# Optimization experiments

Measured on AMD Instinct MI355X. Metric: run time of the kernel, lower is better.

Reference implementation:

```python
import jax, jax.numpy as jnp
import numpy as np

B, D, K = 4096, 1024, 32

def setup_inputs() -> dict:
    key = jax.random.key(0)
    k1, k2, k3, k4 = jax.random.split(key, 4)
    e1 = jax.random.normal(k1, (B, D), dtype=jnp.float32)
    e2 = jax.random.normal(k2, (B, D), dtype=jnp.float32)
    W = jax.random.normal(k3, (K, D, D), dtype=jnp.float32)
    V = jax.random.normal(k4, (2 * D, K), dtype=jnp.float32)
    b = jnp.zeros((D,), dtype=jnp.float32)
    return {"e1": e1, "e2": e2, "W": W, "V": V, "b": b}

def reference(e1, e2, W, V, b):
    batch = e1.shape[0]
    k = W.shape[0]
    # Per-slice bilinear form: btp[i, n] = sum_d e2[n,d] * (e1[n] @ W[i])[d] + sum(b)
    # (b is added elementwise before the axis-1 sum in the original, i.e. +sum(b))
    btp = jnp.einsum('bd,kde,be->kb', e1, W, e2) + jnp.sum(b)  # (k, B)
    # Original concatenates k (B,)-vectors along axis 0 then reshapes to (B, k);
    # reproduce that exact (interleaving) layout.
    btp = btp.reshape(batch, k)
    ff = jnp.concatenate([e1, e2], axis=-1) @ V  # (B, k)
    return jnp.tanh(btp + ff)
```

## Files before the change

kernel.cpp:

```cpp
#include <hip/hip_runtime.h>

#define B_SZ 4096
#define D_SZ 1024
#define K_SZ 32

typedef _Float16 h16x8 __attribute__((ext_vector_type(8)));
typedef float f32x4 __attribute__((ext_vector_type(4)));
typedef float f32x2 __attribute__((ext_vector_type(2)));
typedef unsigned int u32x2 __attribute__((ext_vector_type(2)));
typedef unsigned int u32x4 __attribute__((ext_vector_type(4)));
typedef unsigned short u16x4 __attribute__((ext_vector_type(4)));

#define GLOAD16(gp, sp) __builtin_amdgcn_global_load_lds( \
    (const __attribute__((address_space(1))) void*)(gp),  \
    (__attribute__((address_space(3))) void*)(sp), 16, 0, 0)

__device__ __forceinline__ void split1(float x, _Float16& h, _Float16& l) {
    h = (_Float16)x;
    l = (_Float16)((x - (float)h) * 2048.0f);
}

__global__ __launch_bounds__(256)
void ntl_prep_w(const float* __restrict__ W,
                _Float16* __restrict__ Wh, _Float16* __restrict__ Wl) {
    __shared__ float tile[64 * 69];
    const int bid = blockIdx.x;
    const int k  = bid >> 8;
    const int d0 = ((bid >> 4) & 15) << 6;
    const int e0 = (bid & 15) << 6;
    const int t  = threadIdx.x;
    const int r  = t >> 4;
    const int c4 = (t & 15) << 2;

    const float* src = W + ((size_t)k * D_SZ + d0) * D_SZ + e0;
    #pragma unroll
    for (int p = 0; p < 4; ++p) {
        f32x4 v = *(const f32x4*)(src + (size_t)(p * 16 + r) * D_SZ + c4);
        float* dst = &tile[(p * 16 + r) * 69 + c4];
        dst[0] = v[0]; dst[1] = v[1]; dst[2] = v[2]; dst[3] = v[3];
    }
    __syncthreads();
    #pragma unroll
    for (int p = 0; p < 4; ++p) {
        const int e = p * 16 + r;
        u16x4 hh, ll;
        #pragma unroll
        for (int q = 0; q < 4; ++q) {
            float v = tile[(c4 + q) * 69 + e];
            _Float16 h, l;
            split1(v, h, l);
            hh[q] = __builtin_bit_cast(unsigned short, h);
            ll[q] = __builtin_bit_cast(unsigned short, l);
        }
        const size_t o = ((size_t)k * D_SZ + e0 + e) * D_SZ + d0 + c4;
        *(u16x4*)(Wh + o) = hh;
        *(u16x4*)(Wl + o) = ll;
    }
}

__global__ __launch_bounds__(256)
void ntl_prep_e(const float* __restrict__ e1,
                _Float16* __restrict__ eh, _Float16* __restrict__ el) {
    const size_t i = ((size_t)blockIdx.x * 256 + threadIdx.x) * 4;
    f32x4 v = *(const f32x4*)(e1 + i);
    u16x4 hh, ll;
    #pragma unroll
    for (int q = 0; q < 4; ++q) {
        _Float16 h, l;
        split1(v[q], h, l);
        hh[q] = __builtin_bit_cast(unsigned short, h);
        ll[q] = __builtin_bit_cast(unsigned short, l);
    }
    *(u16x4*)(eh + i) = hh;
    *(u16x4*)(el + i) = ll;
}

__global__ __launch_bounds__(256, 2)
void ntl_bilinear2(const _Float16* __restrict__ eh, const _Float16* __restrict__ el,
                   const _Float16* __restrict__ Wh, const _Float16* __restrict__ Wl,
                   const float* __restrict__ e2, float* __restrict__ out) {
    __shared__ __align__(16) _Float16 lds[4 * 128 * 64];
    char* const base = (char*)lds;

    const int bid = blockIdx.x;
    const int k   = bid >> 8;
    const int rem = bid & 255;
    const int b0  = (rem >> 3) * 128;
    const int e0  = (rem & 7) * 128;

    const int t  = threadIdx.x;
    const int l  = t & 63;
    const int w  = t >> 6;
    const int wr = (w >> 1) * 64;
    const int wc = (w & 1) * 64;
    const int lrow = l & 15;
    const int lq   = l >> 4;

    f32x4 acc1[4][4];
    f32x4 acc2[4][4];
    #pragma unroll
    for (int m = 0; m < 4; ++m)
        #pragma unroll
        for (int n = 0; n < 4; ++n) {
            acc1[m][n] = f32x4{0.f, 0.f, 0.f, 0.f};
            acc2[m][n] = f32x4{0.f, 0.f, 0.f, 0.f};
        }

    const int srow  = l >> 3;
    const int gslot = (l & 7) ^ srow;
    const size_t aoff = (size_t)(b0 + w * 8 + srow) * D_SZ + gslot * 8;
    const size_t boff = ((size_t)k * D_SZ + e0 + w * 8 + srow) * D_SZ + gslot * 8;
    const _Float16* gAh = eh + aoff;
    const _Float16* gAl = el + aoff;
    const _Float16* gBh = Wh + boff;
    const _Float16* gBl = Wl + boff;

    for (int kt = 0; kt < D_SZ / 64; ++kt) {
        const int d0 = kt * 64;
        #pragma unroll
        for (int p = 0; p < 4; ++p) {
            const size_t ro = (size_t)p * 32 * D_SZ + d0;
            char* sb_ = base + p * 4096 + w * 1024;
            GLOAD16(gAh + ro, sb_);
            GLOAD16(gAl + ro, sb_ + 16384);
            GLOAD16(gBh + ro, sb_ + 32768);
            GLOAD16(gBl + ro, sb_ + 49152);
        }
        __syncthreads();

        #pragma unroll
        for (int kk = 0; kk < 2; ++kk) {
            h16x8 a_h[4], a_l[4];
            #pragma unroll
            for (int m = 0; m < 4; ++m) {
                const int r = wr + m * 16 + lrow;
                const int off = r * 128 + (((kk * 4 + lq) ^ (r & 7)) << 4);
                a_h[m] = *(const h16x8*)(base + off);
                a_l[m] = *(const h16x8*)(base + 16384 + off);
            }
            #pragma unroll
            for (int n = 0; n < 4; ++n) {
                const int r = wc + n * 16 + lrow;
                const int off = r * 128 + (((kk * 4 + lq) ^ (r & 7)) << 4);
                h16x8 b_h = *(const h16x8*)(base + 32768 + off);
                h16x8 b_l = *(const h16x8*)(base + 49152 + off);
                #pragma unroll
                for (int m = 0; m < 4; ++m) {
                    acc1[m][n] = __builtin_amdgcn_mfma_f32_16x16x32_f16(a_h[m], b_h, acc1[m][n], 0, 0, 0);
                    acc2[m][n] = __builtin_amdgcn_mfma_f32_16x16x32_f16(a_h[m], b_l, acc2[m][n], 0, 0, 0);
                    acc2[m][n] = __builtin_amdgcn_mfma_f32_16x16x32_f16(a_l[m], b_h, acc2[m][n], 0, 0, 0);
                }
            }
        }
        __syncthreads();
    }

    float rsum[16];
    #pragma unroll
    for (int i = 0; i < 16; ++i) rsum[i] = 0.f;

    #pragma unroll
    for (int m = 0; m < 4; ++m) {
        #pragma unroll
        for (int n = 0; n < 4; ++n) {
            const int col = e0 + wc + n * 16 + lrow;
            #pragma unroll
            for (int j = 0; j < 4; ++j) {
                const int row = b0 + wr + m * 16 + lq * 4 + j;
                float tv = acc1[m][n][j] + acc2[m][n][j] * (1.0f / 2048.0f);
                rsum[m * 4 + j] += tv * e2[(size_t)row * D_SZ + col];
            }
        }
    }

    #pragma unroll
    for (int i = 0; i < 16; ++i) {
        float v = rsum[i];
        v += __shfl_xor(v, 1, 16);
        v += __shfl_xor(v, 2, 16);
        v += __shfl_xor(v, 4, 16);
        v += __shfl_xor(v, 8, 16);
        if (lrow == 0) {
            const int row = b0 + wr + (i >> 2) * 16 + lq * 4 + (i & 3);
            atomicAdd(out + (size_t)k * B_SZ + row, v);
        }
    }
}

__device__ __forceinline__ int swz_fb(int row, int byte_in_row) {
    int slot = byte_in_row >> 4;
    int in   = byte_in_row & 15;
    return row * 128 + (((slot ^ (row & 7)) << 4) | in);
}
__device__ __forceinline__ void split_fb(float x, unsigned short& h, unsigned short& l) {
    _Float16 hf = (_Float16)x;
    float hff = (float)hf;
    _Float16 lf = (_Float16)((x - hff) * 2048.0f);
    h = __builtin_bit_cast(unsigned short, hf);
    l = __builtin_bit_cast(unsigned short, lf);
}
__global__ __launch_bounds__(256, 2)
void ntl_bilinear_fb(const float* __restrict__ e1, const float* __restrict__ e2,
                     const float* __restrict__ W, float* __restrict__ out) {
    __shared__ __align__(16) char smem[65536];
    char* const Ah = smem;
    char* const Al = smem + 16384;
    char* const Bh = smem + 32768;
    char* const Bl = smem + 49152;
    const int bid = blockIdx.x;
    const int k   = bid >> 8;
    const int rem = bid & 255;
    const int b0  = (rem >> 3) * 128;
    const int e0  = (rem & 7) * 128;
    const int t  = threadIdx.x;
    const int l  = t & 63;
    const int w  = t >> 6;
    const int wr = (w >> 1) * 64;
    const int wc = (w & 1) * 64;
    const int lrow = l & 15;
    const int lq   = l >> 4;
    f32x4 acc1[4][4], acc2[4][4];
    #pragma unroll
    for (int m = 0; m < 4; ++m)
        #pragma unroll
        for (int n = 0; n < 4; ++n) {
            acc1[m][n] = f32x4{0.f, 0.f, 0.f, 0.f};
            acc2[m][n] = f32x4{0.f, 0.f, 0.f, 0.f};
        }
    const int sa_row = t >> 4;
    const int sa_cg  = (t & 15) * 4;
    const int sb_e   = t & 127;
    const int sb_dg  = t >> 7;
    const float* const e1b = e1 + (size_t)b0 * D_SZ;
    const float* const wb  = W + ((size_t)k * D_SZ) * D_SZ + e0 + sb_e;
    for (int kt = 0; kt < D_SZ / 64; ++kt) {
        const int d0 = kt * 64;
        #pragma unroll
        for (int p = 0; p < 8; ++p) {
            const int r = sa_row + p * 16;
            f32x4 v = *(const f32x4*)(e1b + (size_t)r * D_SZ + d0 + sa_cg);
            unsigned short hh[4], ll[4];
            #pragma unroll
            for (int q = 0; q < 4; ++q) split_fb(v[q], hh[q], ll[q]);
            u32x2 hv = { (unsigned)hh[0] | ((unsigned)hh[1] << 16),
                         (unsigned)hh[2] | ((unsigned)hh[3] << 16) };
            u32x2 lv = { (unsigned)ll[0] | ((unsigned)ll[1] << 16),
                         (unsigned)ll[2] | ((unsigned)ll[3] << 16) };
            const int ad = swz_fb(r, sa_cg * 2);
            *(u32x2*)(Ah + ad) = hv;
            *(u32x2*)(Al + ad) = lv;
        }
        {
            const float* ws2 = wb + (size_t)(d0 + sb_dg * 32) * D_SZ;
            #pragma unroll
            for (int g = 0; g < 4; ++g) {
                unsigned short hh[8], ll[8];
                #pragma unroll
                for (int i = 0; i < 8; ++i)
                    split_fb(ws2[(size_t)(g * 8 + i) * D_SZ], hh[i], ll[i]);
                u32x4 hv = { (unsigned)hh[0] | ((unsigned)hh[1] << 16),
                             (unsigned)hh[2] | ((unsigned)hh[3] << 16),
                             (unsigned)hh[4] | ((unsigned)hh[5] << 16),
                             (unsigned)hh[6] | ((unsigned)hh[7] << 16) };
                u32x4 lv = { (unsigned)ll[0] | ((unsigned)ll[1] << 16),
                             (unsigned)ll[2] | ((unsigned)ll[3] << 16),
                             (unsigned)ll[4] | ((unsigned)ll[5] << 16),
                             (unsigned)ll[6] | ((unsigned)ll[7] << 16) };
                const int ad = swz_fb(sb_e, (sb_dg * 32 + g * 8) * 2);
                *(u32x4*)(Bh + ad) = hv;
                *(u32x4*)(Bl + ad) = lv;
            }
        }
        __syncthreads();
        #pragma unroll
        for (int kk = 0; kk < 2; ++kk) {
            const int kb = kk * 64 + lq * 16;
            h16x8 a_h[4], a_l[4];
            #pragma unroll
            for (int m = 0; m < 4; ++m) {
                const int ad = swz_fb(wr + m * 16 + lrow, kb);
                a_h[m] = *(const h16x8*)(Ah + ad);
                a_l[m] = *(const h16x8*)(Al + ad);
            }
            #pragma unroll
            for (int n = 0; n < 4; ++n) {
                const int bd = swz_fb(wc + n * 16 + lrow, kb);
                h16x8 b_h = *(const h16x8*)(Bh + bd);
                h16x8 b_l = *(const h16x8*)(Bl + bd);
                #pragma unroll
                for (int m = 0; m < 4; ++m) {
                    acc1[m][n] = __builtin_amdgcn_mfma_f32_16x16x32_f16(a_h[m], b_h, acc1[m][n], 0, 0, 0);
                    acc2[m][n] = __builtin_amdgcn_mfma_f32_16x16x32_f16(a_h[m], b_l, acc2[m][n], 0, 0, 0);
                    acc2[m][n] = __builtin_amdgcn_mfma_f32_16x16x32_f16(a_l[m], b_h, acc2[m][n], 0, 0, 0);
                }
            }
        }
        __syncthreads();
    }
    float rsum[16];
    #pragma unroll
    for (int i = 0; i < 16; ++i) rsum[i] = 0.f;
    #pragma unroll
    for (int m = 0; m < 4; ++m) {
        #pragma unroll
        for (int n = 0; n < 4; ++n) {
            const int col = e0 + wc + n * 16 + lrow;
            #pragma unroll
            for (int j = 0; j < 4; ++j) {
                const int row = b0 + wr + m * 16 + lq * 4 + j;
                float tv = acc1[m][n][j] + acc2[m][n][j] * (1.0f / 2048.0f);
                rsum[m * 4 + j] += tv * e2[(size_t)row * D_SZ + col];
            }
        }
    }
    #pragma unroll
    for (int i = 0; i < 16; ++i) {
        float v = rsum[i];
        v += __shfl_xor(v, 1, 16);
        v += __shfl_xor(v, 2, 16);
        v += __shfl_xor(v, 4, 16);
        v += __shfl_xor(v, 8, 16);
        if (lrow == 0) {
            const int row = b0 + wr + (i >> 2) * 16 + lq * 4 + (i & 3);
            atomicAdd(out + (size_t)k * B_SZ + row, v);
        }
    }
}

__global__ __launch_bounds__(256)
void ntl_ff(const float* __restrict__ e1, const float* __restrict__ e2,
            const float* __restrict__ V, float* __restrict__ out) {
    __shared__ float vt[32 * 258];
    const int t  = threadIdx.x;
    const int c  = t & 31;
    const int rl = t >> 5;
    const int r  = blockIdx.x * 8 + rl;
    float acc = 0.f;
    for (int j0 = 0; j0 < 2 * D_SZ; j0 += 256) {
        __syncthreads();
        #pragma unroll
        for (int i = 0; i < 32; ++i) {
            const int f = i * 256 + t;
            vt[(f & 31) * 258 + (f >> 5)] = V[(size_t)j0 * K_SZ + f];
        }
        __syncthreads();
        const float* src = (j0 < D_SZ) ? (e1 + (size_t)r * D_SZ + j0)
                                       : (e2 + (size_t)r * D_SZ + (j0 - D_SZ));
        #pragma unroll 8
        for (int jj = 0; jj < 256; jj += 2) {
            f32x2 a  = *(const f32x2*)(src + jj);
            f32x2 vv = *(const f32x2*)(&vt[c * 258 + jj]);
            acc += a[0] * vv[0] + a[1] * vv[1];
        }
    }
    out[(size_t)r * K_SZ + c] += acc;
}

__global__ void ntl_sumb(const float* __restrict__ b, float* __restrict__ ws) {
    __shared__ float red[256];
    const int t = threadIdx.x;
    red[t] = b[t] + b[t + 256] + b[t + 512] + b[t + 768];
    __syncthreads();
    for (int s = 128; s > 0; s >>= 1) {
        if (t < s) red[t] += red[t + s];
        __syncthreads();
    }
    if (t == 0) ws[0] = red[0];
}

__global__ void ntl_tanh(float* __restrict__ out, const float* __restrict__ ws) {
    const int p = blockIdx.x * 256 + threadIdx.x;
    out[p] = tanhf(out[p] + ws[0]);
}

extern "C" void kernel_launch(void* const* d_in, const int* in_sizes, int n_in,
                              void* d_out, int out_size, void* d_ws, size_t ws_size,
                              hipStream_t stream) {
    const float* e1 = (const float*)d_in[0];
    const float* e2 = (const float*)d_in[1];
    const float* W  = (const float*)d_in[2];
    const float* V  = (const float*)d_in[3];
    const float* b  = (const float*)d_in[4];
    float* out = (float*)d_out;

    const size_t WT = (size_t)K_SZ * D_SZ * D_SZ;
    const size_t ET = (size_t)B_SZ * D_SZ;
    const size_t need = (2 * WT + 2 * ET) * sizeof(_Float16) + 16;

    hipMemsetAsync(d_out, 0, (size_t)B_SZ * K_SZ * sizeof(float), stream);

    if (ws_size >= need) {
        _Float16* Wh = (_Float16*)d_ws;
        _Float16* Wl = Wh + WT;
        _Float16* eh = Wl + WT;
        _Float16* el = eh + ET;
        float* sb = (float*)(el + ET);
        ntl_sumb<<<1, 256, 0, stream>>>(b, sb);
        ntl_prep_w<<<dim3(K_SZ * 256), dim3(256), 0, stream>>>(W, Wh, Wl);
        ntl_prep_e<<<dim3((int)(ET / 1024)), dim3(256), 0, stream>>>(e1, eh, el);
        ntl_bilinear2<<<dim3(K_SZ * 256), dim3(256), 0, stream>>>(eh, el, Wh, Wl, e2, out);
        ntl_ff<<<dim3(B_SZ / 8), dim3(256), 0, stream>>>(e1, e2, V, out);
        ntl_tanh<<<dim3((B_SZ * K_SZ) / 256), dim3(256), 0, stream>>>(out, sb);
    } else {
        float* sb = (float*)d_ws;
        ntl_sumb<<<1, 256, 0, stream>>>(b, sb);
        ntl_bilinear_fb<<<dim3(K_SZ * 256), dim3(256), 0, stream>>>(e1, e2, W, out);
        ntl_ff<<<dim3(B_SZ / 8), dim3(256), 0, stream>>>(e1, e2, V, out);
        ntl_tanh<<<dim3((B_SZ * K_SZ) / 256), dim3(256), 0, stream>>>(out, sb);
    }
}
```

Measured before the change: 820.2 us.

## Rewrite bilinear GEMM with 256x128 tiles, 32x32 MFMA and double-buffered prefetch

Replaces the 128x128, 256-thread bilinear kernel with a 512-thread kernel. Each block computes a 256x128 tile using 32x32x16 MFMA instructions. B tiles are double-buffered in LDS through direct global-to-LDS loads, and the next A tile is prefetched into registers while the current step computes. Blocks are also remapped so that each XCD works on a fixed range of batch rows, which should improve L2 reuse. The aim is to cut global traffic per FLOP and hide load latency, at the cost of a 128 KB LDS footprint that likely allows only one block per CU.

```diff
diff --git a/kernel.cpp b/kernel.cpp
--- a/kernel.cpp
+++ b/kernel.cpp
@@ -3,8 +3,10 @@
 #define B_SZ 4096
 #define D_SZ 1024
 #define K_SZ 32
+#define NT   16
 
 typedef _Float16 h16x8 __attribute__((ext_vector_type(8)));
+typedef float f32x16 __attribute__((ext_vector_type(16)));
 typedef float f32x4 __attribute__((ext_vector_type(4)));
 typedef float f32x2 __attribute__((ext_vector_type(2)));
 typedef unsigned int u32x2 __attribute__((ext_vector_type(2)));
@@ -75,114 +77,162 @@
     *(u16x4*)(el + i) = ll;
 }
 
-__global__ __launch_bounds__(256, 2)
-void ntl_bilinear2(const _Float16* __restrict__ eh, const _Float16* __restrict__ el,
+__global__ __launch_bounds__(512, 2)
+void ntl_bilinear4(const _Float16* __restrict__ eh, const _Float16* __restrict__ el,
                    const _Float16* __restrict__ Wh, const _Float16* __restrict__ Wl,
                    const float* __restrict__ e2, float* __restrict__ out) {
-    __shared__ __align__(16) _Float16 lds[4 * 128 * 64];
-    char* const base = (char*)lds;
-
-    const int bid = blockIdx.x;
-    const int k   = bid >> 8;
-    const int rem = bid & 255;
-    const int b0  = (rem >> 3) * 128;
-    const int e0  = (rem & 7) * 128;
-
-    const int t  = threadIdx.x;
-    const int l  = t & 63;
-    const int w  = t >> 6;
-    const int wr = (w >> 1) * 64;
-    const int wc = (w & 1) * 64;
-    const int lrow = l & 15;
-    const int lq   = l >> 4;
-
-    f32x4 acc1[4][4];
-    f32x4 acc2[4][4];
-    #pragma unroll
-    for (int m = 0; m < 4; ++m)
-        #pragma unroll
-        for (int n = 0; n < 4; ++n) {
-            acc1[m][n] = f32x4{0.f, 0.f, 0.f, 0.f};
-            acc2[m][n] = f32x4{0.f, 0.f, 0.f, 0.f};
-        }
-
-    const int srow  = l >> 3;
-    const int gslot = (l & 7) ^ srow;
-    const size_t aoff = (size_t)(b0 + w * 8 + srow) * D_SZ + gslot * 8;
-    const size_t boff = ((size_t)k * D_SZ + e0 + w * 8 + srow) * D_SZ + gslot * 8;
-    const _Float16* gAh = eh + aoff;
-    const _Float16* gAl = el + aoff;
-    const _Float16* gBh = Wh + boff;
-    const _Float16* gBl = Wl + boff;
-
-    for (int kt = 0; kt < D_SZ / 64; ++kt) {
-        const int d0 = kt * 64;
-        #pragma unroll
-        for (int p = 0; p < 4; ++p) {
-            const size_t ro = (size_t)p * 32 * D_SZ + d0;
-            char* sb_ = base + p * 4096 + w * 1024;
-            GLOAD16(gAh + ro, sb_);
-            GLOAD16(gAl + ro, sb_ + 16384);
-            GLOAD16(gBh + ro, sb_ + 32768);
-            GLOAD16(gBl + ro, sb_ + 49152);
-        }
-        __syncthreads();
-
-        #pragma unroll
-        for (int kk = 0; kk < 2; ++kk) {
-            h16x8 a_h[4], a_l[4];
-            #pragma unroll
-            for (int m = 0; m < 4; ++m) {
-                const int r = wr + m * 16 + lrow;
-                const int off = r * 128 + (((kk * 4 + lq) ^ (r & 7)) << 4);
-                a_h[m] = *(const h16x8*)(base + off);
-                a_l[m] = *(const h16x8*)(base + 16384 + off);
-            }
-            #pragma unroll
-            for (int n = 0; n < 4; ++n) {
-                const int r = wc + n * 16 + lrow;
-                const int off = r * 128 + (((kk * 4 + lq) ^ (r & 7)) << 4);
-                h16x8 b_h = *(const h16x8*)(base + 32768 + off);
-                h16x8 b_l = *(const h16x8*)(base + 49152 + off);
+    __shared__ __align__(16) char lds[131072];
+
+    const int bid   = blockIdx.x;
+    const int xcd   = bid & 7;
+    const int idx   = bid >> 3;
+    const int e_t   = idx & 7;
+    const int b_sub = (idx >> 3) & 1;
+    const int k     = idx >> 4;
+    const int b0    = (xcd * 2 + b_sub) * 256;
+    const int e0    = e_t * 128;
+
+    const int t    = threadIdx.x;
+    const int l    = t & 63;
+    const int w    = t >> 6;
+    const int wrow = (w >> 1) * 64;
+    const int wcol = (w & 1) * 64;
+    const int l31  = l & 31;
+    const int h5   = l >> 5;
+    const int srow = l >> 3;
+    const int sl   = l & 7;
+
+    f32x16 acc1[2][2];
+    f32x16 acc2[2][2];
+    #pragma unroll
+    for (int m = 0; m < 2; ++m)
+        #pragma unroll
+        for (int n = 0; n < 2; ++n) {
+            #pragma unroll
+            for (int j = 0; j < 16; ++j) { acc1[m][n][j] = 0.f; acc2[m][n][j] = 0.f; }
+        }
+
+    const size_t arow = (size_t)(b0 + w * 32 + srow) * D_SZ + sl * 8;
+    const _Float16* gAh = eh + arow;
+    const _Float16* gAl = el + arow;
+    const int awOff = (w * 32 + srow) * 128 + ((sl ^ srow) << 4);
+
+    const int gslot = sl ^ srow;
+    const _Float16* gB = (w < 4 ? Wh : Wl) +
+        ((size_t)k * D_SZ + e0 + (w & 3) * 32 + srow) * D_SZ + gslot * 8;
+    const int bOff = (w >= 4 ? 16384 : 0) + (w & 3) * 4096;
+
+    u32x4 arH[4], arL[4];
+
+    {
+        char* bset = lds + 65536;
+        #pragma unroll
+        for (int i = 0; i < 4; ++i)
+            GLOAD16(gB + (size_t)i * 8 * D_SZ, bset + bOff + i * 1024);
+        #pragma unroll
+        for (int i = 0; i < 4; ++i) {
+            arH[i] = *(const u32x4*)(gAh + (size_t)i * 8 * D_SZ);
+            arL[i] = *(const u32x4*)(gAl + (size_t)i * 8 * D_SZ);
+        }
+    }
+
+    for (int kt = 0; kt < NT; ++kt) {
+        if (kt) {
+            __builtin_amdgcn_s_barrier();
+            __builtin_amdgcn_sched_barrier(0);
+        }
+        asm volatile("s_waitcnt vmcnt(0)" ::: "memory");
+        __builtin_amdgcn_sched_barrier(0);
+
+        #pragma unroll
+        for (int i = 0; i < 4; ++i) {
+            *(u32x4*)(lds + awOff + i * 1024)         = arH[i];
+            *(u32x4*)(lds + 32768 + awOff + i * 1024) = arL[i];
+        }
+
+        if (kt + 1 < NT) {
+            const size_t dn = (size_t)(kt + 1) * 64;
+            char* bset = lds + 65536 + (((kt + 1) & 1) << 15);
+            #pragma unroll
+            for (int i = 0; i < 4; ++i)
+                GLOAD16(gB + (size_t)i * 8 * D_SZ + dn, bset + bOff + i * 1024);
+            #pragma unroll
+            for (int i = 0; i < 4; ++i) {
+                arH[i] = *(const u32x4*)(gAh + (size_t)i * 8 * D_SZ + dn);
+                arL[i] = *(const u32x4*)(gAl + (size_t)i * 8 * D_SZ + dn);
+            }
+        }
+
+        asm volatile("s_waitcnt lgkmcnt(0)" ::: "memory");
+        __builtin_amdgcn_sched_barrier(0);
+        __builtin_amdgcn_s_barrier();
+        __builtin_amdgcn_sched_barrier(0);
+
+        const char* Bh_ = lds + 65536 + ((kt & 1) << 15);
+        const char* Bl_ = Bh_ + 16384;
+
+        #pragma unroll
+        for (int ks = 0; ks < 4; ++ks) {
+            h16x8 ah[2], al[2], bh[2], bl[2];
+            #pragma unroll
+            for (int m = 0; m < 2; ++m) {
+                const int r = wrow + m * 32 + l31;
+                const int off = r * 128 + (((ks * 2 + h5) ^ (r & 7)) << 4);
+                ah[m] = *(const h16x8*)(lds + off);
+                al[m] = *(const h16x8*)(lds + 32768 + off);
+            }
+            #pragma unroll
+            for (int n = 0; n < 2; ++n) {
+                const int r = wcol + n * 32 + l31;
+                const int off = r * 128 + (((ks * 2 + h5) ^ (r & 7)) << 4);
+                bh[n] = *(const h16x8*)(Bh_ + off);
+                bl[n] = *(const h16x8*)(Bl_ + off);
+            }
+            #pragma unroll
+            for (int m = 0; m < 2; ++m)
                 #pragma unroll
-                for (int m = 0; m < 4; ++m) {
-                    acc1[m][n] = __builtin_amdgcn_mfma_f32_16x16x32_f16(a_h[m], b_h, acc1[m][n], 0, 0, 0);
-                    acc2[m][n] = __builtin_amdgcn_mfma_f32_16x16x32_f16(a_h[m], b_l, acc2[m][n], 0, 0, 0);
-                    acc2[m][n] = __builtin_amdgcn_mfma_f32_16x16x32_f16(a_l[m], b_h, acc2[m][n], 0, 0, 0);
+                for (int n = 0; n < 2; ++n) {
+                    acc1[m][n] = __builtin_amdgcn_mfma_f32_32x32x16_f16(ah[m], bh[n], acc1[m][n], 0, 0, 0);
+                    acc2[m][n] = __builtin_amdgcn_mfma_f32_32x32x16_f16(ah[m], bl[n], acc2[m][n], 0, 0, 0);
+                    acc2[m][n] = __builtin_amdgcn_mfma_f32_32x32x16_f16(al[m], bh[n], acc2[m][n], 0, 0, 0);
                 }
-            }
-        }
-        __syncthreads();
-    }
-
-    float rsum[16];
-    #pragma unroll
-    for (int i = 0; i < 16; ++i) rsum[i] = 0.f;
-
-    #pragma unroll
-    for (int m = 0; m < 4; ++m) {
-        #pragma unroll
-        for (int n = 0; n < 4; ++n) {
-            const int col = e0 + wc + n * 16 + lrow;
-            #pragma unroll
-            for (int j = 0; j < 4; ++j) {
-                const int row = b0 + wr + m * 16 + lq * 4 + j;
-                float tv = acc1[m][n][j] + acc2[m][n][j] * (1.0f / 2048.0f);
-                rsum[m * 4 + j] += tv * e2[(size_t)row * D_SZ + col];
-            }
-        }
-    }
-
-    #pragma unroll
-    for (int i = 0; i < 16; ++i) {
-        float v = rsum[i];
-        v += __shfl_xor(v, 1, 16);
-        v += __shfl_xor(v, 2, 16);
-        v += __shfl_xor(v, 4, 16);
-        v += __shfl_xor(v, 8, 16);
-        if (lrow == 0) {
-            const int row = b0 + wr + (i >> 2) * 16 + lq * 4 + (i & 3);
-            atomicAdd(out + (size_t)k * B_SZ + row, v);
+        }
+    }
+
+    float rsum[2][16];
+    #pragma unroll
+    for (int m = 0; m < 2; ++m)
+        #pragma unroll
+        for (int rg = 0; rg < 16; ++rg) rsum[m][rg] = 0.f;
+
+    #pragma unroll
+    for (int m = 0; m < 2; ++m) {
+        #pragma unroll
+        for (int n = 0; n < 2; ++n) {
+            #pragma unroll
+            for (int rg = 0; rg < 16; ++rg) {
+                const int rowl = wrow + m * 32 + (rg & 3) + 8 * (rg >> 2) + 4 * h5;
+                const int col  = e0 + wcol + n * 32 + l31;
+                float tv = acc1[m][n][rg] + acc2[m][n][rg] * (1.0f / 2048.0f);
+                rsum[m][rg] += tv * e2[(size_t)(b0 + rowl) * D_SZ + col];
+            }
+        }
+    }
+
+    #pragma unroll
+    for (int m = 0; m < 2; ++m) {
+        #pragma unroll
+        for (int rg = 0; rg < 16; ++rg) {
+            float v = rsum[m][rg];
+            v += __shfl_xor(v, 1, 32);
+            v += __shfl_xor(v, 2, 32);
+            v += __shfl_xor(v, 4, 32);
+            v += __shfl_xor(v, 8, 32);
+            v += __shfl_xor(v, 16, 32);
+            if (l31 == 0) {
+                const int rowl = wrow + m * 32 + (rg & 3) + 8 * (rg >> 2) + 4 * h5;
+                atomicAdd(out + (size_t)k * B_SZ + b0 + rowl, v);
+            }
         }
     }
 }
@@ -233,7 +283,7 @@
     const int sb_dg  = t >> 7;
     const float* const e1b = e1 + (size_t)b0 * D_SZ;
     const float* const wb  = W + ((size_t)k * D_SZ) * D_SZ + e0 + sb_e;
-    for (int kt = 0; kt < D_SZ / 64; ++kt) {
+    for (int kt = 0; kt < NT; ++kt) {
         const int d0 = kt * 64;
         #pragma unroll
         for (int p = 0; p < 8; ++p) {
@@ -241,7 +291,7 @@
             f32x4 v = *(const f32x4*)(e1b + (size_t)r * D_SZ + d0 + sa_cg);
             unsigned short hh[4], ll[4];
             #pragma unroll
-            for (int q = 0; q < 4; ++q) split_fb(v[q], hh[q], ll[q]);
+            for (int qq = 0; qq < 4; ++qq) split_fb(v[qq], hh[qq], ll[qq]);
             u32x2 hv = { (unsigned)hh[0] | ((unsigned)hh[1] << 16),
                          (unsigned)hh[2] | ((unsigned)hh[3] << 16) };
             u32x2 lv = { (unsigned)ll[0] | ((unsigned)ll[1] << 16),
@@ -253,11 +303,11 @@
         {
             const float* ws2 = wb + (size_t)(d0 + sb_dg * 32) * D_SZ;
             #pragma unroll
-            for (int g = 0; g < 4; ++g) {
+            for (int gg = 0; gg < 4; ++gg) {
                 unsigned short hh[8], ll[8];
                 #pragma unroll
                 for (int i = 0; i < 8; ++i)
-                    split_fb(ws2[(size_t)(g * 8 + i) * D_SZ], hh[i], ll[i]);
+                    split_fb(ws2[(size_t)(gg * 8 + i) * D_SZ], hh[i], ll[i]);
                 u32x4 hv = { (unsigned)hh[0] | ((unsigned)hh[1] << 16),
                              (unsigned)hh[2] | ((unsigned)hh[3] << 16),
                              (unsigned)hh[4] | ((unsigned)hh[5] << 16),
@@ -266,7 +316,7 @@
                              (unsigned)ll[2] | ((unsigned)ll[3] << 16),
                              (unsigned)ll[4] | ((unsigned)ll[5] << 16),
                              (unsigned)ll[6] | ((unsigned)ll[7] << 16) };
-                const int ad = swz_fb(sb_e, (sb_dg * 32 + g * 8) * 2);
+                const int ad = swz_fb(sb_e, (sb_dg * 32 + gg * 8) * 2);
                 *(u32x4*)(Bh + ad) = hv;
                 *(u32x4*)(Bl + ad) = lv;
             }
@@ -398,7 +448,7 @@
         ntl_sumb<<<1, 256, 0, stream>>>(b, sb);
         ntl_prep_w<<<dim3(K_SZ * 256), dim3(256), 0, stream>>>(W, Wh, Wl);
         ntl_prep_e<<<dim3((int)(ET / 1024)), dim3(256), 0, stream>>>(e1, eh, el);
-        ntl_bilinear2<<<dim3(K_SZ * 256), dim3(256), 0, stream>>>(eh, el, Wh, Wl, e2, out);
+        ntl_bilinear4<<<dim3(4096), dim3(512), 0, stream>>>(eh, el, Wh, Wl, e2, out);
         ntl_ff<<<dim3(B_SZ / 8), dim3(256), 0, stream>>>(e1, e2, V, out);
         ntl_tanh<<<dim3((B_SZ * K_SZ) / 256), dim3(256), 0, stream>>>(out, sb);
     } else {
```

After: 947.0 us. 1.15x slower.

## Double-buffer LDS in bilinear GEMM with 32-wide K tiles and async prefetch

Applied to the files above, without the earlier changes.

Replaces the single-buffered 64-wide K-step loop with a double-buffered pipeline over 32-wide K tiles. Each LDS row now packs the hi and lo halves together, and the next-but-one tile is prefetched while the current one is computed, using manual vmcnt waits and raw s_barriers. The aim is to overlap global-to-LDS loads with MFMA work instead of stalling on __syncthreads every step. In exchange it doubles the number of barriers and iterations. The hand-tuned waitcnt must match the exact number of outstanding loads, or the pipeline will read data that has not arrived yet.

```diff
diff --git a/kernel.cpp b/kernel.cpp
--- a/kernel.cpp
+++ b/kernel.cpp
@@ -3,6 +3,7 @@
 #define B_SZ 4096
 #define D_SZ 1024
 #define K_SZ 32
+#define NT   32
 
 typedef _Float16 h16x8 __attribute__((ext_vector_type(8)));
 typedef float f32x4 __attribute__((ext_vector_type(4)));
@@ -76,11 +77,10 @@
 }
 
 __global__ __launch_bounds__(256, 2)
-void ntl_bilinear2(const _Float16* __restrict__ eh, const _Float16* __restrict__ el,
+void ntl_bilinear6(const _Float16* __restrict__ eh, const _Float16* __restrict__ el,
                    const _Float16* __restrict__ Wh, const _Float16* __restrict__ Wl,
                    const float* __restrict__ e2, float* __restrict__ out) {
-    __shared__ __align__(16) _Float16 lds[4 * 128 * 64];
-    char* const base = (char*)lds;
+    __shared__ __align__(16) char lds[65536];
 
     const int bid = blockIdx.x;
     const int k   = bid >> 8;
@@ -106,54 +106,93 @@
             acc2[m][n] = f32x4{0.f, 0.f, 0.f, 0.f};
         }
 
-    const int srow  = l >> 3;
-    const int gslot = (l & 7) ^ srow;
-    const size_t aoff = (size_t)(b0 + w * 8 + srow) * D_SZ + gslot * 8;
-    const size_t boff = ((size_t)k * D_SZ + e0 + w * 8 + srow) * D_SZ + gslot * 8;
-    const _Float16* gAh = eh + aoff;
-    const _Float16* gAl = el + aoff;
-    const _Float16* gBh = Wh + boff;
-    const _Float16* gBl = Wl + boff;
-
-    for (int kt = 0; kt < D_SZ / 64; ++kt) {
-        const int d0 = kt * 64;
-        #pragma unroll
-        for (int p = 0; p < 4; ++p) {
-            const size_t ro = (size_t)p * 32 * D_SZ + d0;
-            char* sb_ = base + p * 4096 + w * 1024;
-            GLOAD16(gAh + ro, sb_);
-            GLOAD16(gAl + ro, sb_ + 16384);
-            GLOAD16(gBh + ro, sb_ + 32768);
-            GLOAD16(gBl + ro, sb_ + 49152);
-        }
-        __syncthreads();
-
-        #pragma unroll
-        for (int kk = 0; kk < 2; ++kk) {
-            h16x8 a_h[4], a_l[4];
+    const int sline = l >> 3;
+    const int sx    = (l & 7) ^ sline;
+    const int hl    = sx >> 2;
+    const int lqs   = sx & 3;
+
+    const _Float16* aBase = hl ? el : eh;
+    const _Float16* bBase = hl ? Wl : Wh;
+    const _Float16* gA[4];
+    const _Float16* gB[4];
+    #pragma unroll
+    for (int i = 0; i < 4; ++i) {
+        const int row = w * 32 + i * 8 + sline;
+        gA[i] = aBase + (size_t)(b0 + row) * D_SZ + lqs * 8;
+        gB[i] = bBase + ((size_t)k * D_SZ + e0 + row) * D_SZ + lqs * 8;
+    }
+    const int sOff = w * 32 * 128;
+
+#define STAGE(bufsel, ktv) do {                                          \
+        char* bb = lds + ((bufsel) ? 32768 : 0);                         \
+        const size_t kb = (size_t)(ktv) * 32;                            \
+        GLOAD16(gA[0] + kb, bb + sOff);                                  \
+        GLOAD16(gA[1] + kb, bb + sOff + 1024);                           \
+        GLOAD16(gA[2] + kb, bb + sOff + 2048);                           \
+        GLOAD16(gA[3] + kb, bb + sOff + 3072);                           \
+        GLOAD16(gB[0] + kb, bb + 16384 + sOff);                          \
+        GLOAD16(gB[1] + kb, bb + 16384 + sOff + 1024);                   \
+        GLOAD16(gB[2] + kb, bb + 16384 + sOff + 2048);                   \
+        GLOAD16(gB[3] + kb, bb + 16384 + sOff + 3072);                   \
+    } while (0)
+
+    int aoffH[4], aoffL[4], boffH[4], boffL[4];
+    #pragma unroll
+    for (int m = 0; m < 4; ++m) {
+        const int r = wr + m * 16 + lrow;
+        aoffH[m] = r * 128 + ((lq       ^ (r & 7)) << 4);
+        aoffL[m] = r * 128 + (((4 | lq) ^ (r & 7)) << 4);
+    }
+    #pragma unroll
+    for (int n = 0; n < 4; ++n) {
+        const int r = wc + n * 16 + lrow;
+        boffH[n] = 16384 + r * 128 + ((lq       ^ (r & 7)) << 4);
+        boffL[n] = 16384 + r * 128 + (((4 | lq) ^ (r & 7)) << 4);
+    }
+
+    STAGE(0, 0);
+    STAGE(1, 1);
+
+    for (int kt = 0; kt < NT; ++kt) {
+        if (kt < NT - 1) {
+            asm volatile("s_waitcnt vmcnt(8)" ::: "memory");
+        } else {
+            asm volatile("s_waitcnt vmcnt(0)" ::: "memory");
+        }
+        __builtin_amdgcn_sched_barrier(0);
+        __builtin_amdgcn_s_barrier();
+        __builtin_amdgcn_sched_barrier(0);
+
+        const char* buf = lds + ((kt & 1) ? 32768 : 0);
+
+        h16x8 a_h[4], a_l[4];
+        #pragma unroll
+        for (int m = 0; m < 4; ++m) {
+            a_h[m] = *(const h16x8*)(buf + aoffH[m]);
+            a_l[m] = *(const h16x8*)(buf + aoffL[m]);
+        }
+        #pragma unroll
+        for (int n = 0; n < 4; ++n) {
+            h16x8 b_h = *(const h16x8*)(buf + boffH[n]);
+            h16x8 b_l = *(const h16x8*)(buf + boffL[n]);
             #pragma unroll
             for (int m = 0; m < 4; ++m) {
-                const int r = wr + m * 16 + lrow;
-                const int off = r * 128 + (((kk * 4 + lq) ^ (r & 7)) << 4);
-                a_h[m] = *(const h16x8*)(base + off);
-                a_l[m] = *(const h16x8*)(base + 16384 + off);
-            }
-            #pragma unroll
-            for (int n = 0; n < 4; ++n) {
-                const int r = wc + n * 16 + lrow;
-                const int off = r * 128 + (((kk * 4 + lq) ^ (r & 7)) << 4);
-                h16x8 b_h = *(const h16x8*)(base + 32768 + off);
-                h16x8 b_l = *(const h16x8*)(base + 49152 + off);
-                #pragma unroll
-                for (int m = 0; m < 4; ++m) {
-                    acc1[m][n] = __builtin_amdgcn_mfma_f32_16x16x32_f16(a_h[m], b_h, acc1[m][n], 0, 0, 0);
-                    acc2[m][n] = __builtin_amdgcn_mfma_f32_16x16x32_f16(a_h[m], b_l, acc2[m][n], 0, 0, 0);
-                    acc2[m][n] = __builtin_amdgcn_mfma_f32_16x16x32_f16(a_l[m], b_h, acc2[m][n], 0, 0, 0);
-                }
-            }
-        }
-        __syncthreads();
-    }
+                acc1[m][n] = __builtin_amdgcn_mfma_f32_16x16x32_f16(a_h[m], b_h, acc1[m][n], 0, 0, 0);
+                acc2[m][n] = __builtin_amdgcn_mfma_f32_16x16x32_f16(a_h[m], b_l, acc2[m][n], 0, 0, 0);
+                acc2[m][n] = __builtin_amdgcn_mfma_f32_16x16x32_f16(a_l[m], b_h, acc2[m][n], 0, 0, 0);
+            }
+        }
+
+        __builtin_amdgcn_sched_barrier(0);
+        __builtin_amdgcn_s_barrier();
+        __builtin_amdgcn_sched_barrier(0);
+
+        if (kt + 2 < NT) {
+            STAGE(kt & 1, kt + 2);
+            __builtin_amdgcn_sched_barrier(0);
+        }
+    }
+#undef STAGE
 
     float rsum[16];
     #pragma unroll
@@ -233,15 +272,15 @@
     const int sb_dg  = t >> 7;
     const float* const e1b = e1 + (size_t)b0 * D_SZ;
     const float* const wb  = W + ((size_t)k * D_SZ) * D_SZ + e0 + sb_e;
-    for (int kt = 0; kt < D_SZ / 64; ++kt) {
+    for (int kt = 0; kt < 16; ++kt) {
         const int d0 = kt * 64;
         #pragma unroll
         for (int p = 0; p < 8; ++p) {
             const int r = sa_row + p * 16;
-            f32x4 v = *(const f32x4*)(e1b + (size_t)r * D_SZ + d0 + sa_cg);
+            f32x4 vv4 = *(const f32x4*)(e1b + (size_t)r * D_SZ + d0 + sa_cg);
             unsigned short hh[4], ll[4];
             #pragma unroll
-            for (int q = 0; q < 4; ++q) split_fb(v[q], hh[q], ll[q]);
+            for (int qq = 0; qq < 4; ++qq) split_fb(vv4[qq], hh[qq], ll[qq]);
             u32x2 hv = { (unsigned)hh[0] | ((unsigned)hh[1] << 16),
                          (unsigned)hh[2] | ((unsigned)hh[3] << 16) };
             u32x2 lv = { (unsigned)ll[0] | ((unsigned)ll[1] << 16),
@@ -253,11 +292,11 @@
         {
             const float* ws2 = wb + (size_t)(d0 + sb_dg * 32) * D_SZ;
             #pragma unroll
-            for (int g = 0; g < 4; ++g) {
+            for (int gg = 0; gg < 4; ++gg) {
                 unsigned short hh[8], ll[8];
                 #pragma unroll
                 for (int i = 0; i < 8; ++i)
-                    split_fb(ws2[(size_t)(g * 8 + i) * D_SZ], hh[i], ll[i]);
+                    split_fb(ws2[(size_t)(gg * 8 + i) * D_SZ], hh[i], ll[i]);
                 u32x4 hv = { (unsigned)hh[0] | ((unsigned)hh[1] << 16),
                              (unsigned)hh[2] | ((unsigned)hh[3] << 16),
                              (unsigned)hh[4] | ((unsigned)hh[5] << 16),
@@ -266,7 +305,7 @@
                              (unsigned)ll[2] | ((unsigned)ll[3] << 16),
                              (unsigned)ll[4] | ((unsigned)ll[5] << 16),
                              (unsigned)ll[6] | ((unsigned)ll[7] << 16) };
-                const int ad = swz_fb(sb_e, (sb_dg * 32 + g * 8) * 2);
+                const int ad = swz_fb(sb_e, (sb_dg * 32 + gg * 8) * 2);
                 *(u32x4*)(Bh + ad) = hv;
                 *(u32x4*)(Bl + ad) = lv;
             }
@@ -306,23 +345,23 @@
         for (int n = 0; n < 4; ++n) {
             const int col = e0 + wc + n * 16 + lrow;
             #pragma unroll
-            for (int j = 0; j < 4; ++j) {
-                const int row = b0 + wr + m * 16 + lq * 4 + j;
-                float tv = acc1[m][n][j] + acc2[m][n][j] * (1.0f / 2048.0f);
-                rsum[m * 4 + j] += tv * e2[(size_t)row * D_SZ + col];
+            for (int jq = 0; jq < 4; ++jq) {
+                const int row = b0 + wr + m * 16 + lq * 4 + jq;
+                float tv = acc1[m][n][jq] + acc2[m][n][jq] * (1.0f / 2048.0f);
+                rsum[m * 4 + jq] += tv * e2[(size_t)row * D_SZ + col];
             }
         }
     }
     #pragma unroll
     for (int i = 0; i < 16; ++i) {
-        float v = rsum[i];
-        v += __shfl_xor(v, 1, 16);
-        v += __shfl_xor(v, 2, 16);
-        v += __shfl_xor(v, 4, 16);
-        v += __shfl_xor(v, 8, 16);
+        float vv = rsum[i];
+        vv += __shfl_xor(vv, 1, 16);
+        vv += __shfl_xor(vv, 2, 16);
+        vv += __shfl_xor(vv, 4, 16);
+        vv += __shfl_xor(vv, 8, 16);
         if (lrow == 0) {
             const int row = b0 + wr + (i >> 2) * 16 + lq * 4 + (i & 3);
-            atomicAdd(out + (size_t)k * B_SZ + row, v);
+            atomicAdd(out + (size_t)k * B_SZ + row, vv);
         }
     }
 }
@@ -392,13 +431,13 @@
     if (ws_size >= need) {
         _Float16* Wh = (_Float16*)d_ws;
         _Float16* Wl = Wh + WT;
-        _Float16* eh = Wl + WT;
-        _Float16* el = eh + ET;
-        float* sb = (float*)(el + ET);
+        _Float16* ehp = Wl + WT;
+        _Float16* elp = ehp + ET;
+        float* sb = (float*)(elp + ET);
         ntl_sumb<<<1, 256, 0, stream>>>(b, sb);
         ntl_prep_w<<<dim3(K_SZ * 256), dim3(256), 0, stream>>>(W, Wh, Wl);
-        ntl_prep_e<<<dim3((int)(ET / 1024)), dim3(256), 0, stream>>>(e1, eh, el);
-        ntl_bilinear2<<<dim3(K_SZ * 256), dim3(256), 0, stream>>>(eh, el, Wh, Wl, e2, out);
+        ntl_prep_e<<<dim3((int)(ET / 1024)), dim3(256), 0, stream>>>(e1, ehp, elp);
+        ntl_bilinear6<<<dim3(K_SZ * 256), dim3(256), 0, stream>>>(ehp, elp, Wh, Wl, e2, out);
         ntl_ff<<<dim3(B_SZ / 8), dim3(256), 0, stream>>>(e1, e2, V, out);
         ntl_tanh<<<dim3((B_SZ * K_SZ) / 256), dim3(256), 0, stream>>>(out, sb);
     } else {
```

New measurement: 920.3 us. 1.12x slower.
